# Performance work log

Hardware: AMD Instinct MI355X
Metric: run time of the kernel (lower is better)

The kernel has to match this reference:

```python
import jax, jax.numpy as jnp
import numpy as np

EPS = 1e-5

def conv(x, w, stride=1, pad=0, groups=1):
    # x: NCHW, w: OIHW
    return jax.lax.conv_general_dilated(
        x, w, window_strides=(stride, stride),
        padding=[(pad, pad), (pad, pad)],
        dimension_numbers=("NCHW", "OIHW", "NCHW"),
        feature_group_count=groups)

def bn_eval(x, gamma, beta, mean, var):
    scale = (gamma / jnp.sqrt(var + EPS))[None, :, None, None]
    shift = (beta - mean * gamma / jnp.sqrt(var + EPS))[None, :, None, None]
    return x * scale + shift

def setup_inputs() -> dict:
    key = jax.random.key(0)
    ks = jax.random.split(key, 12)
    B, Cin, H, W = 32, 64, 56, 56
    hidden, red, Cout, K = 384, 16, 64, 3
    f32 = jnp.float32
    x = jax.random.normal(ks[0], (B, Cin, H, W), dtype=f32)
    w_exp = jax.random.normal(ks[1], (hidden, Cin, 3, 3), dtype=f32) * 0.05
    w_dw  = jax.random.normal(ks[2], (hidden, 1, K, K), dtype=f32) * 0.1
    w_se1 = jax.random.normal(ks[3], (red, hidden, 1, 1), dtype=f32) * 0.05
    w_se2 = jax.random.normal(ks[4], (hidden, red, 1, 1), dtype=f32) * 0.1
    w_pw  = jax.random.normal(ks[5], (Cout, hidden, 1, 1), dtype=f32) * 0.05
    def bn_params(k, c):
        k1, k2 = jax.random.split(k)
        return (jnp.ones((c,), f32), jnp.zeros((c,), f32),
                jax.random.normal(k1, (c,), dtype=f32) * 0.01,
                jax.random.uniform(k2, (c,), dtype=f32, minval=0.5, maxval=1.5))
    g1, b1, m1, v1 = bn_params(ks[6], hidden)
    g2, b2, m2, v2 = bn_params(ks[7], hidden)
    g3, b3, m3, v3 = bn_params(ks[8], Cout)
    return dict(x=x, w_exp=w_exp, g1=g1, b1=b1, m1=m1, v1=v1,
                w_dw=w_dw, g2=g2, b2=b2, m2=m2, v2=v2,
                w_se1=w_se1, w_se2=w_se2, w_pw=w_pw,
                g3=g3, b3=b3, m3=m3, v3=v3)

def reference(x, w_exp, g1, b1, m1, v1, w_dw, g2, b2, m2, v2,
              w_se1, w_se2, w_pw, g3, b3, m3, v3):
    hidden = w_exp.shape[0]
    # expand conv (3x3) + BN + SiLU
    h = jax.nn.silu(bn_eval(conv(x, w_exp, stride=1, pad=1), g1, b1, m1, v1))
    # depthwise conv + BN + SiLU
    d = jax.nn.silu(bn_eval(conv(h, w_dw, stride=1, pad=1, groups=hidden), g2, b2, m2, v2))
    # squeeze-excitation: global avg pool -> 1x1 -> SiLU -> 1x1 -> sigmoid -> scale
    s = jnp.mean(d, axis=(2, 3), keepdims=True)            # [B, hidden, 1, 1]
    s = jax.nn.silu(conv(s, w_se1))
    s = jax.nn.sigmoid(conv(s, w_se2))
    d = d * s
    # pointwise projection + BN
    y = bn_eval(conv(d, w_pw), g3, b3, m3, v3)
    # eval mode: stochastic_depth is identity; quant_skip == (identity-quantized) input
    return y + x
```

## Files before the change

kernel.cpp:

```cpp
#include <hip/hip_runtime.h>

typedef unsigned short u16;
typedef unsigned int u32;
typedef __attribute__((ext_vector_type(2))) u32 u32x2;
typedef __attribute__((ext_vector_type(4))) u32 u32x4;
typedef __attribute__((ext_vector_type(4))) float f32x4;
typedef __attribute__((ext_vector_type(8))) short s16x8;

#define DEV __device__ __forceinline__

DEV float bflo(u32 u){ union{u32 i; float f;} c; c.i = u << 16; return c.f; }
DEV float bfhi(u32 u){ union{u32 i; float f;} c; c.i = u & 0xffff0000u; return c.f; }
DEV u16 f2b(float f){
  union{float f; u32 u;} c; c.f = f;
  u32 u = c.u;
  u32 r = (u + 0x7fffu + ((u >> 16) & 1u)) >> 16;
  return (u16)r;
}
DEV float fsilu(float v){ return v / (1.f + __expf(-v)); }

typedef const __attribute__((address_space(1))) u32 gu32;
typedef __attribute__((address_space(3))) u32 lu32;
DEV void gload16(const u32* g, u32* l) {
  __builtin_amdgcn_global_load_lds((gu32*)g, (lu32*)l, 16, 0, 0);
}

constexpr int Bn = 32, Cin = 64, H = 56, Wd = 56, HID = 384, CO = 64;
constexpr int HW = H * Wd;
constexpr float EPS = 1e-5f;

constexpr int XROW = 72 * 64;
constexpr int WTAP = 128 * 64;
constexpr int WOCT = 9 * WTAP;
constexpr int XTROW = 72 * 64;

__global__ __launch_bounds__(256) void k_prep_wbn(
    const float* __restrict__ w,
    const float* __restrict__ g1, const float* __restrict__ b1,
    const float* __restrict__ m1, const float* __restrict__ v1,
    const float* __restrict__ g3, const float* __restrict__ b3,
    const float* __restrict__ m3, const float* __restrict__ v3,
    u16* __restrict__ wt,
    float* __restrict__ sc1, float* __restrict__ sh1,
    float* __restrict__ sc3, float* __restrict__ sh3)
{
  const int blk = blockIdx.x;
  if (blk < 864) {
    int t = blk * 256 + threadIdx.x;
    int octile = t / WOCT, r = t - octile * WOCT;
    int tap = r / WTAP, r2 = r - tap * WTAP;
    int ocl = r2 >> 6, col = r2 & 63;
    int physo = col >> 3, j = col & 7;
    int olog = physo ^ (ocl & 7);
    int ic = olog * 8 + j;
    int oc = octile * 128 + ocl;
    wt[t] = f2b(w[(oc * Cin + ic) * 9 + tap]);
  } else {
    for (int t = threadIdx.x; t < HID; t += 256) {
      float sc = g1[t] * rsqrtf(v1[t] + EPS);
      sc1[t] = sc;
      sh1[t] = b1[t] - m1[t] * sc;
    }
    if (threadIdx.x < CO) {
      int t = threadIdx.x;
      float sc = g3[t] * rsqrtf(v3[t] + EPS);
      sc3[t] = sc;
      sh3[t] = b3[t] - m3[t] * sc;
    }
  }
}

__global__ __launch_bounds__(256) void k_prep_x(
    const float* __restrict__ x, u16* __restrict__ xt, int b0)
{
  const int row = blockIdx.x;
  const int b = blockIdx.y, gb = b0 + b;
  const int tid = threadIdx.x;
  u16* dst = xt + ((size_t)b * 58 + row) * XTROW;
  if (row == 0 || row == 57) {
    for (int i = tid; i < 2304; i += 256) ((u32*)dst)[i] = 0;
    return;
  }
  const int y = row - 1;
  __shared__ u16 sx[64 * 58];
  {
    const int ic = tid >> 2, seg = tid & 3;
    const float* xp = x + ((size_t)(gb * Cin + ic) * H + y) * Wd + seg * 14;
    #pragma unroll
    for (int t = 0; t < 14; ++t) sx[ic * 58 + seg * 14 + t] = f2b(xp[t]);
  }
  __syncthreads();
  #pragma unroll
  for (int it = 0; it < 18; ++it) {
    const int slot = it * 4 + (tid >> 6);
    const int j = tid & 63;
    u16 v = 0;
    if (slot >= 1 && slot <= 56) {
      int ic = (((j >> 3) ^ (slot & 7)) << 3) | (j & 7);
      v = sx[ic * 58 + (slot - 1)];
    }
    dst[slot * 64 + j] = v;
  }
}

__global__ __launch_bounds__(256, 2) void k_expand_mfma(
    const u16* __restrict__ xt, const u16* __restrict__ wt,
    const float* __restrict__ sc1, const float* __restrict__ sh1,
    u16* __restrict__ h, int b0)
{
  (void)b0;
  __shared__ u16 sB[4 * XROW];
  __shared__ u16 sA[2][WTAP];
  const int tid = threadIdx.x;
  const int ypair = blockIdx.x, b = blockIdx.y;
  const int y0 = ypair * 2;
  const int wave = tid >> 6, ln = tid & 63;
  const int wm = wave >> 1, wn = wave & 1;
  const int lane15 = ln & 15, quad = ln >> 4;

  {
    const u32* xsrc = (const u32*)(xt + ((size_t)b * 58 + y0) * XTROW);
    #pragma unroll
    for (int it = 0; it < 9; ++it) {
      int chunk = it * 256 + tid;
      gload16(xsrc + chunk * 4, (u32*)sB + (chunk & ~63) * 4);
    }
    const u32* wsrc = (const u32*)wt;
    #pragma unroll
    for (int it = 0; it < 4; ++it) {
      int chunk = it * 256 + tid;
      gload16(wsrc + chunk * 4, (u32*)sA[0] + (chunk & ~63) * 4);
    }
  }
  __syncthreads();

  const int y = y0 + wn;

  f32x4 acc[4][4];
  #pragma unroll
  for (int ms = 0; ms < 4; ++ms)
    #pragma unroll
    for (int ns = 0; ns < 4; ++ns) acc[ms][ns] = (f32x4){0.f, 0.f, 0.f, 0.f};

  int buf = 0;
  int octile = 0, tap = 0;
  for (int step = 0; step < 27; ++step) {
    if (step < 26) {
      const u32* wsrc = (const u32*)(wt + (size_t)(step + 1) * WTAP);
      u32* sAn = (u32*)sA[buf ^ 1];
      #pragma unroll
      for (int it = 0; it < 4; ++it) {
        int chunk = it * 256 + tid;
        gload16(wsrc + chunk * 4, sAn + (chunk & ~63) * 4);
      }
    }

    const int dy = tap / 3, dx = tap - dy * 3;
    const u16* sAc = sA[buf];
    #pragma unroll
    for (int kk = 0; kk < 2; ++kk) {
      s16x8 af[4], bf[4];
      #pragma unroll
      for (int ms = 0; ms < 4; ++ms) {
        int ocl = wm * 64 + ms * 16 + lane15;
        int po = (kk * 4 + quad) ^ (ocl & 7);
        af[ms] = *(const s16x8*)&sAc[ocl * 64 + po * 8];
      }
      #pragma unroll
      for (int ns = 0; ns < 4; ++ns) {
        int row = wn + dy;
        int slot = ns * 16 + lane15 + dx;
        int po = (kk * 4 + quad) ^ (slot & 7);
        bf[ns] = *(const s16x8*)&sB[(row * 72 + slot) * 64 + po * 8];
      }
      #pragma unroll
      for (int ms = 0; ms < 4; ++ms)
        #pragma unroll
        for (int ns = 0; ns < 4; ++ns)
          acc[ms][ns] = __builtin_amdgcn_mfma_f32_16x16x32_bf16(
              af[ms], bf[ns], acc[ms][ns], 0, 0, 0);
    }

    __syncthreads();
    buf ^= 1;

    if (++tap == 9) {
      #pragma unroll
      for (int ms = 0; ms < 4; ++ms) {
        int oc0 = octile * 128 + wm * 64 + ms * 16 + quad * 4;
        f32x4 sc = *(const f32x4*)&sc1[oc0];
        f32x4 sh = *(const f32x4*)&sh1[oc0];
        float scr[4] = {sc.x, sc.y, sc.z, sc.w};
        float shr[4] = {sh.x, sh.y, sh.z, sh.w};
        #pragma unroll
        for (int ns = 0; ns < 4; ++ns) {
          int xg = ns * 16 + lane15;
          if (xg < Wd) {
            float av[4] = {acc[ms][ns].x, acc[ms][ns].y, acc[ms][ns].z, acc[ms][ns].w};
            #pragma unroll
            for (int r = 0; r < 4; ++r) {
              float val = fsilu(av[r] * scr[r] + shr[r]);
              h[((size_t)(b * HID + oc0 + r) * H + y) * Wd + xg] = f2b(val);
            }
          }
        }
      }
      #pragma unroll
      for (int ms = 0; ms < 4; ++ms)
        #pragma unroll
        for (int ns = 0; ns < 4; ++ns) acc[ms][ns] = (f32x4){0.f, 0.f, 0.f, 0.f};
      tap = 0;
      ++octile;
    }
  }
}

__global__ __launch_bounds__(256) void k_dw(
    const u16* __restrict__ h, const float* __restrict__ wdw,
    const float* __restrict__ g2, const float* __restrict__ b2,
    const float* __restrict__ m2, const float* __restrict__ v2,
    u16* __restrict__ d, float* __restrict__ mean)
{
  __shared__ float red[4];
  const int tid = threadIdx.x;
  const int c = blockIdx.x, b = blockIdx.y;
  const u32* hp32 = (const u32*)(h + (size_t)(b * HID + c) * HW);

  float wv[9];
  #pragma unroll
  for (int t = 0; t < 9; ++t) wv[t] = wdw[c * 9 + t];
  const float sc = g2[c] * rsqrtf(v2[c] + EPS);
  const float sh = b2[c] - m2[c] * sc;

  float lsum = 0.f;
  if (tid < 224) {
    const int row = tid >> 2, seg = tid & 3;
    const int px0 = seg * 14, w0 = px0 >> 1;

    float v[3][16];
    #pragma unroll
    for (int r3 = 0; r3 < 3; ++r3) {
      int rr = row + r3 - 1;
      bool ok = (rr >= 0) && (rr < 56);
      const u32* rp = hp32 + rr * 28;
      v[r3][0] = (ok && seg > 0) ? bfhi(rp[w0 - 1]) : 0.f;
      #pragma unroll
      for (int t = 0; t < 7; ++t) {
        u32 wd = ok ? rp[w0 + t] : 0u;
        v[r3][1 + 2 * t] = bflo(wd);
        v[r3][2 + 2 * t] = bfhi(wd);
      }
      v[r3][15] = (ok && seg < 3) ? bflo(rp[w0 + 7]) : 0.f;
    }

    u32 pk[7];
    #pragma unroll
    for (int t = 0; t < 7; ++t) {
      float o2[2];
      #pragma unroll
      for (int e = 0; e < 2; ++e) {
        int j = 2 * t + e;
        float s = 0.f;
        #pragma unroll
        for (int r3 = 0; r3 < 3; ++r3)
          #pragma unroll
          for (int dx = 0; dx < 3; ++dx)
            s += v[r3][j + dx] * wv[r3 * 3 + dx];
        float val = fsilu(s * sc + sh);
        lsum += val;
        o2[e] = val;
      }
      pk[t] = (u32)f2b(o2[0]) | ((u32)f2b(o2[1]) << 16);
    }
    u32* dp32 = (u32*)(d + (size_t)(b * HID + c) * HW) + row * 28 + w0;
    #pragma unroll
    for (int t = 0; t < 7; ++t) dp32[t] = pk[t];
  }

  #pragma unroll
  for (int off = 32; off > 0; off >>= 1) lsum += __shfl_down(lsum, off);
  if ((tid & 63) == 0) red[tid >> 6] = lsum;
  __syncthreads();
  if (tid == 0)
    mean[b * HID + c] = (red[0] + red[1] + red[2] + red[3]) * (1.f / 3136.f);
}

constexpr int PWP = 392;

__global__ __launch_bounds__(256, 2) void k_pw_mfma(
    const u16* __restrict__ d, const float* __restrict__ mean,
    const float* __restrict__ w1, const float* __restrict__ w2,
    const float* __restrict__ wpw,
    const float* __restrict__ sc3, const float* __restrict__ sh3,
    const float* __restrict__ x, float* __restrict__ out, int b0)
{
  __shared__ u16 sAw[64 * PWP];
  __shared__ u32 dtw[4 * 1024];
  __shared__ float smn[HID];
  __shared__ float sps[16 * 17];
  __shared__ float ss1[16];
  __shared__ float ssf[HID];
  const int tid = threadIdx.x;
  const int b = blockIdx.y, gb = b0 + b;
  const int p0 = blockIdx.x * 256;
  const int wave = tid >> 6, ln = tid & 63;
  const int lane15 = ln & 15, quad = ln >> 4;

  for (int c = tid; c < HID; c += 256) smn[c] = mean[b * HID + c];
  __syncthreads();
  {
    int r = tid >> 4, j = tid & 15;
    float p = 0.f;
    for (int c = j; c < HID; c += 16) p += smn[c] * w1[r * HID + c];
    sps[r * 17 + j] = p;
  }
  __syncthreads();
  if (tid < 16) {
    float s = 0.f;
    #pragma unroll
    for (int q = 0; q < 16; ++q) s += sps[tid * 17 + q];
    ss1[tid] = fsilu(s);
  }
  __syncthreads();
  for (int c = tid; c < HID; c += 256) {
    float s = 0.f;
    #pragma unroll
    for (int q = 0; q < 16; ++q) s += ss1[q] * w2[c * 16 + q];
    ssf[c] = 1.f / (1.f + __expf(-s));
  }
  __syncthreads();

  {
    for (int i = tid; i < 6144; i += 256) {
      int e = i * 4, co = e / 384, k = e - co * 384;
      f32x4 wv = *(const f32x4*)&wpw[e];
      f32x4 sf = *(const f32x4*)&ssf[k];
      float s3 = sc3[co];
      u32x2 pk;
      pk.x = (u32)f2b(wv.x * sf.x * s3) | ((u32)f2b(wv.y * sf.y * s3) << 16);
      pk.y = (u32)f2b(wv.z * sf.z * s3) | ((u32)f2b(wv.w * sf.w * s3) << 16);
      *(u32x2*)&sAw[co * PWP + k] = pk;
    }
  }
  __syncthreads();

  f32x4 acc[4][4];
  #pragma unroll
  for (int ms = 0; ms < 4; ++ms)
    #pragma unroll
    for (int ns = 0; ns < 4; ++ns) acc[ms][ns] = (f32x4){0.f, 0.f, 0.f, 0.f};

  const int cpair8 = ln >> 3;
  const int pxo = (ln & 7) * 8;
  const int swz = ln & 3;
  const int pbase = p0 + wave * 64;
  u32* mydt = &dtw[wave * 1024];
  const bool ld_ok = (pbase + pxo + 8 <= HW);
  const u16* dbase = d + (size_t)b * HID * HW + pbase + pxo;

  u32x4 pr0[2], pr1[2];
  #pragma unroll
  for (int ci = 0; ci < 2; ++ci) {
    pr0[ci] = (u32x4){0,0,0,0}; pr1[ci] = (u32x4){0,0,0,0};
    if (ld_ok) {
      int c = 2 * (ci * 8 + cpair8);
      const u16* dpp = dbase + (size_t)c * HW;
      pr0[ci] = *(const u32x4*)dpp;
      pr1[ci] = *(const u32x4*)(dpp + HW);
    }
  }

  for (int ks = 0; ks < 12; ++ks) {
    #pragma unroll
    for (int ci = 0; ci < 2; ++ci) {
      int k4 = ci * 2 + (cpair8 >> 2);
      u32* w0 = &mydt[pxo * 16 + ((k4 ^ swz) << 2) + (cpair8 & 3)];
      u32x4 r0 = pr0[ci], r1 = pr1[ci];
      w0[0 * 16] = (r0.x & 0xffffu) | (r1.x << 16);
      w0[1 * 16] = (r0.x >> 16)     | (r1.x & 0xffff0000u);
      w0[2 * 16] = (r0.y & 0xffffu) | (r1.y << 16);
      w0[3 * 16] = (r0.y >> 16)     | (r1.y & 0xffff0000u);
      w0[4 * 16] = (r0.z & 0xffffu) | (r1.z << 16);
      w0[5 * 16] = (r0.z >> 16)     | (r1.z & 0xffff0000u);
      w0[6 * 16] = (r0.w & 0xffffu) | (r1.w << 16);
      w0[7 * 16] = (r0.w >> 16)     | (r1.w & 0xffff0000u);
    }
    if (ks < 11) {
      #pragma unroll
      for (int ci = 0; ci < 2; ++ci) {
        if (ld_ok) {
          int c = (ks + 1) * 32 + 2 * (ci * 8 + cpair8);
          const u16* dpp = dbase + (size_t)c * HW;
          pr0[ci] = *(const u32x4*)dpp;
          pr1[ci] = *(const u32x4*)(dpp + HW);
        }
      }
    }
    const int k0 = ks * 32;
    s16x8 af[4], bf[4];
    #pragma unroll
    for (int ms = 0; ms < 4; ++ms) {
      int ocl = ms * 16 + lane15;
      af[ms] = *(const s16x8*)&sAw[ocl * PWP + k0 + quad * 8];
    }
    #pragma unroll
    for (int ns = 0; ns < 4; ++ns) {
      int pxl = ns * 16 + lane15;
      int p4 = quad ^ ((pxl >> 3) & 3);
      bf[ns] = *(const s16x8*)((const u16*)mydt + pxl * 32 + p4 * 8);
    }
    #pragma unroll
    for (int ms = 0; ms < 4; ++ms)
      #pragma unroll
      for (int ns = 0; ns < 4; ++ns)
        acc[ms][ns] = __builtin_amdgcn_mfma_f32_16x16x32_bf16(
            af[ms], bf[ns], acc[ms][ns], 0, 0, 0);
  }

  #pragma unroll
  for (int ns = 0; ns < 4; ++ns) {
    int p = pbase + ns * 16 + lane15;
    if (p < HW) {
      #pragma unroll
      for (int ms = 0; ms < 4; ++ms) {
        int co0 = ms * 16 + quad * 4;
        float av[4] = {acc[ms][ns].x, acc[ms][ns].y, acc[ms][ns].z, acc[ms][ns].w};
        #pragma unroll
        for (int r = 0; r < 4; ++r) {
          size_t idx = (size_t)(gb * CO + co0 + r) * HW + p;
          out[idx] = av[r] + sh3[co0 + r] + x[idx];
        }
      }
    }
  }
}

extern "C" void kernel_launch(void* const* d_in, const int* in_sizes, int n_in,
                              void* d_out, int out_size, void* d_ws, size_t ws_size,
                              hipStream_t stream)
{
  (void)in_sizes; (void)n_in; (void)out_size;
  const float* x     = (const float*)d_in[0];
  const float* w_exp = (const float*)d_in[1];
  const float* g1 = (const float*)d_in[2];
  const float* b1 = (const float*)d_in[3];
  const float* m1 = (const float*)d_in[4];
  const float* v1 = (const float*)d_in[5];
  const float* w_dw = (const float*)d_in[6];
  const float* g2 = (const float*)d_in[7];
  const float* b2 = (const float*)d_in[8];
  const float* m2 = (const float*)d_in[9];
  const float* v2 = (const float*)d_in[10];
  const float* w_se1 = (const float*)d_in[11];
  const float* w_se2 = (const float*)d_in[12];
  const float* w_pw  = (const float*)d_in[13];
  const float* g3 = (const float*)d_in[14];
  const float* b3 = (const float*)d_in[15];
  const float* m3 = (const float*)d_in[16];
  const float* v3 = (const float*)d_in[17];

  const size_t perB = (size_t)HID * HW * 2 * 2 + HID * 4 + (size_t)58 * XTROW * 2;
  const size_t fixed = 221184 * 2 + HID * 8 + CO * 8;
  int bc = Bn;
  while (bc > 1 && fixed + (size_t)bc * perB > ws_size) bc >>= 1;

  u16* wt = (u16*)d_ws;
  float* sc1 = (float*)(wt + 221184);
  float* sh1 = sc1 + HID;
  float* sc3 = sh1 + HID;
  float* sh3 = sc3 + CO;
  u16* h  = (u16*)(sh3 + CO);
  u16* dd = h + (size_t)bc * HID * HW;
  float* mean = (float*)(dd + (size_t)bc * HID * HW);
  u16* xt = (u16*)(mean + (size_t)bc * HID);

  k_prep_wbn<<<865, 256, 0, stream>>>(w_exp, g1, b1, m1, v1, g3, b3, m3, v3,
                                      wt, sc1, sh1, sc3, sh3);

  for (int b0 = 0; b0 < Bn; b0 += bc) {
    k_prep_x<<<dim3(58, bc), 256, 0, stream>>>(x, xt, b0);
    k_expand_mfma<<<dim3(28, bc), 256, 0, stream>>>(xt, wt, sc1, sh1, h, b0);
    k_dw<<<dim3(HID, bc), 256, 0, stream>>>(h, w_dw, g2, b2, m2, v2, dd, mean);
    k_pw_mfma<<<dim3(13, bc), 256, 0, stream>>>(dd, mean, w_se1, w_se2, w_pw,
                                                sc3, sh3, x, (float*)d_out, b0);
  }
}
```

Baseline: 278.5 us.

## Register-prefetch expand weights, raise MFMA priority, and restructure depthwise conv

In the expand conv, the next tap's weights are now fetched with ordinary global loads into registers before the MFMA loop and written to LDS after it, replacing the direct global-to-LDS async loads. The MFMA section runs at raised wave priority. The depthwise kernel is rewritten so each thread handles a 2-pixel column over 7 rows with a sliding 3-row window, packed f32x2 FMAs and a hardware bf16 pack instruction. The goals are overlapping weight loads with compute, fewer redundant row loads in depthwise, and cheaper arithmetic, at the cost of extra registers in the MFMA kernel and a different global memory access pattern.

```diff
diff --git a/kernel.cpp b/kernel.cpp
--- a/kernel.cpp
+++ b/kernel.cpp
@@ -4,6 +4,7 @@
 typedef unsigned int u32;
 typedef __attribute__((ext_vector_type(2))) u32 u32x2;
 typedef __attribute__((ext_vector_type(4))) u32 u32x4;
+typedef __attribute__((ext_vector_type(2))) float f32x2;
 typedef __attribute__((ext_vector_type(4))) float f32x4;
 typedef __attribute__((ext_vector_type(8))) short s16x8;
 
@@ -145,18 +146,19 @@
   int buf = 0;
   int octile = 0, tap = 0;
   for (int step = 0; step < 27; ++step) {
-    if (step < 26) {
-      const u32* wsrc = (const u32*)(wt + (size_t)(step + 1) * WTAP);
-      u32* sAn = (u32*)sA[buf ^ 1];
-      #pragma unroll
-      for (int it = 0; it < 4; ++it) {
-        int chunk = it * 256 + tid;
-        gload16(wsrc + chunk * 4, sAn + (chunk & ~63) * 4);
-      }
+    u32x4 pf0, pf1, pf2, pf3;
+    const bool pre = (step < 26);
+    if (pre) {
+      const u16* wnx = wt + (size_t)(step + 1) * WTAP;
+      pf0 = *(const u32x4*)&wnx[(0 * 256 + tid) * 8];
+      pf1 = *(const u32x4*)&wnx[(1 * 256 + tid) * 8];
+      pf2 = *(const u32x4*)&wnx[(2 * 256 + tid) * 8];
+      pf3 = *(const u32x4*)&wnx[(3 * 256 + tid) * 8];
     }
 
     const int dy = tap / 3, dx = tap - dy * 3;
     const u16* sAc = sA[buf];
+    __builtin_amdgcn_s_setprio(1);
     #pragma unroll
     for (int kk = 0; kk < 2; ++kk) {
       s16x8 af[4], bf[4];
@@ -180,7 +182,15 @@
           acc[ms][ns] = __builtin_amdgcn_mfma_f32_16x16x32_bf16(
               af[ms], bf[ns], acc[ms][ns], 0, 0, 0);
     }
-
+    __builtin_amdgcn_s_setprio(0);
+
+    if (pre) {
+      u16* sAn = sA[buf ^ 1];
+      *(u32x4*)&sAn[(0 * 256 + tid) * 8] = pf0;
+      *(u32x4*)&sAn[(1 * 256 + tid) * 8] = pf1;
+      *(u32x4*)&sAn[(2 * 256 + tid) * 8] = pf2;
+      *(u32x4*)&sAn[(3 * 256 + tid) * 8] = pf3;
+    }
     __syncthreads();
     buf ^= 1;
 
@@ -226,55 +236,63 @@
   const int c = blockIdx.x, b = blockIdx.y;
   const u32* hp32 = (const u32*)(h + (size_t)(b * HID + c) * HW);
 
-  float wv[9];
-  #pragma unroll
-  for (int t = 0; t < 9; ++t) wv[t] = wdw[c * 9 + t];
+  f32x2 wv2[9];
+  #pragma unroll
+  for (int t = 0; t < 9; ++t) {
+    float w = wdw[c * 9 + t];
+    wv2[t] = (f32x2){w, w};
+  }
   const float sc = g2[c] * rsqrtf(v2[c] + EPS);
   const float sh = b2[c] - m2[c] * sc;
+  const f32x2 scv = (f32x2){sc, sc}, shv = (f32x2){sh, sh};
 
   float lsum = 0.f;
   if (tid < 224) {
-    const int row = tid >> 2, seg = tid & 3;
-    const int px0 = seg * 14, w0 = px0 >> 1;
-
-    float v[3][16];
-    #pragma unroll
-    for (int r3 = 0; r3 < 3; ++r3) {
-      int rr = row + r3 - 1;
-      bool ok = (rr >= 0) && (rr < 56);
-      const u32* rp = hp32 + rr * 28;
-      v[r3][0] = (ok && seg > 0) ? bfhi(rp[w0 - 1]) : 0.f;
-      #pragma unroll
-      for (int t = 0; t < 7; ++t) {
-        u32 wd = ok ? rp[w0 + t] : 0u;
-        v[r3][1 + 2 * t] = bflo(wd);
-        v[r3][2 + 2 * t] = bfhi(wd);
+    const int r7 = tid / 28;
+    const int wd = tid - r7 * 28;
+    const int r0 = r7 * 7;
+    u32* dp32 = (u32*)(d + (size_t)(b * HID + c) * HW);
+
+    auto loadrow = [&](int rr, f32x2* P) {
+      u32 m = 0, c0 = 0, p = 0;
+      if (rr >= 0 && rr < 56) {
+        const u32* rp = hp32 + rr * 28;
+        c0 = rp[wd];
+        if (wd > 0)  m = rp[wd - 1];
+        if (wd < 27) p = rp[wd + 1];
       }
-      v[r3][15] = (ok && seg < 3) ? bflo(rp[w0 + 7]) : 0.f;
-    }
-
-    u32 pk[7];
-    #pragma unroll
-    for (int t = 0; t < 7; ++t) {
-      float o2[2];
-      #pragma unroll
-      for (int e = 0; e < 2; ++e) {
-        int j = 2 * t + e;
-        float s = 0.f;
-        #pragma unroll
-        for (int r3 = 0; r3 < 3; ++r3)
-          #pragma unroll
-          for (int dx = 0; dx < 3; ++dx)
-            s += v[r3][j + dx] * wv[r3 * 3 + dx];
-        float val = fsilu(s * sc + sh);
-        lsum += val;
-        o2[e] = val;
-      }
-      pk[t] = (u32)f2b(o2[0]) | ((u32)f2b(o2[1]) << 16);
-    }
-    u32* dp32 = (u32*)(d + (size_t)(b * HID + c) * HW) + row * 28 + w0;
-    #pragma unroll
-    for (int t = 0; t < 7; ++t) dp32[t] = pk[t];
+      float f_hm = bfhi(m), f_lc = bflo(c0), f_hc = bfhi(c0), f_lp = bflo(p);
+      P[0] = (f32x2){f_hm, f_lc};
+      P[1] = (f32x2){f_lc, f_hc};
+      P[2] = (f32x2){f_hc, f_lp};
+    };
+
+    f32x2 Pa[3], Pb[3], Pc[3];
+    loadrow(r0 - 1, Pa);
+    loadrow(r0,     Pb);
+    f32x2 ls2 = (f32x2){0.f, 0.f};
+    #pragma unroll
+    for (int i = 0; i < 7; ++i) {
+      loadrow(r0 + i + 1, Pc);
+      f32x2 s = (f32x2){0.f, 0.f};
+      #pragma unroll
+      for (int dx = 0; dx < 3; ++dx) s = __builtin_elementwise_fma(Pa[dx], wv2[dx], s);
+      #pragma unroll
+      for (int dx = 0; dx < 3; ++dx) s = __builtin_elementwise_fma(Pb[dx], wv2[3 + dx], s);
+      #pragma unroll
+      for (int dx = 0; dx < 3; ++dx) s = __builtin_elementwise_fma(Pc[dx], wv2[6 + dx], s);
+      f32x2 t = __builtin_elementwise_fma(s, scv, shv);
+      f32x2 val;
+      val.x = fsilu(t.x);
+      val.y = fsilu(t.y);
+      ls2 += val;
+      u32 pk;
+      asm("v_cvt_pk_bf16_f32 %0, %1, %2" : "=v"(pk) : "v"(val.x), "v"(val.y));
+      dp32[(r0 + i) * 28 + wd] = pk;
+      #pragma unroll
+      for (int q = 0; q < 3; ++q) { Pa[q] = Pb[q]; Pb[q] = Pc[q]; }
+    }
+    lsum = ls2.x + ls2.y;
   }
 
   #pragma unroll
```

Result: faster. 267.1 us (-4.1%).
